# Kernel optimization log

Measured on AMD Instinct MI355X. Metric: run time of the kernel, lower is better.

## Reference

```python
import jax, jax.numpy as jnp
import numpy as np

B, S, D, H = 4, 1024, 1024, 16
DH = D // H


def setup_inputs() -> dict:
    key = jax.random.key(0)
    ks = jax.random.split(key, 9)
    s = 0.02
    return {
        "x": jax.random.normal(ks[0], (B, S, D), dtype=jnp.float32),
        "mask": jax.random.randint(ks[1], (B, 1, S), 0, 2, dtype=jnp.int32),
        "Wq": jax.random.normal(ks[2], (D, D), dtype=jnp.float32) * s,
        "bq": jnp.zeros((D,), dtype=jnp.float32),
        "Wk": jax.random.normal(ks[3], (D, D), dtype=jnp.float32) * s,
        "Wv": jax.random.normal(ks[4], (D, D), dtype=jnp.float32) * s,
        "bv": jnp.zeros((D,), dtype=jnp.float32),
        "Wo": jax.random.normal(ks[5], (D, D), dtype=jnp.float32) * s,
        "bo": jnp.zeros((D,), dtype=jnp.float32),
    }


def reference(x, mask, Wq, bq, Wk, Wv, bv, Wo, bo):
    # Linear projections (torch Linear: y = x @ W.T + b)
    q = x @ Wq.T + bq
    k = x @ Wk.T  # key has bias=False
    v = x @ Wv.T + bv

    scale = jnp.asarray(DH, x.dtype) ** (-0.25)
    # [B,S,D] -> [B,H,S,DH]
    qh = q.reshape(B, S, H, DH).transpose(0, 2, 1, 3) * scale
    kh = k.reshape(B, S, H, DH).transpose(0, 2, 1, 3) * scale
    vh = v.reshape(B, S, H, DH).transpose(0, 2, 1, 3)

    qk = jnp.einsum("bhqd,bhkd->bhqk", qh, kh)  # [B,H,S,S]

    # pad-mask branch: mask [B,1,S] -> [B,1,1,S], 0 means padded
    pad = (mask == 0)[:, :, None, :]
    min_value = jnp.finfo(qk.dtype).min
    qk = jnp.where(pad, min_value, qk)

    qk = qk.astype(jnp.float32)
    w = jax.nn.softmax(qk, axis=-1).astype(x.dtype)
    w = jnp.where(pad, jnp.asarray(0.0, w.dtype), w)

    wv = jnp.einsum("bhqk,bhkd->bhqd", w, vh)  # [B,H,S,DH]
    wv = wv.transpose(0, 2, 1, 3).reshape(B, S, D)
    out = wv @ Wo.T + bo
    return out, jax.lax.stop_gradient(qk)
```

## Files before the change

### kernel.cpp

```cpp
#include <hip/hip_runtime.h>

#define NB 4
#define NS 1024
#define ND 1024
#define NH 16
#define NDH 64

typedef __attribute__((ext_vector_type(8))) short short8;
typedef __attribute__((ext_vector_type(4))) short s16x4;
typedef __attribute__((ext_vector_type(4))) float f32x4;

#define SENT (-3.3895313892515355e38f)

static __device__ __forceinline__ unsigned short f2bf(float f) {
    unsigned u = __builtin_bit_cast(unsigned, f);
    u += 0x7fffu + ((u >> 16) & 1u);
    return (unsigned short)(u >> 16);
}

static __device__ __forceinline__ f32x4 mfma16(short8 a, short8 b, f32x4 c) {
    return __builtin_amdgcn_mfma_f32_16x16x32_bf16(a, b, c, 0, 0, 0);
}

typedef const __attribute__((address_space(1))) unsigned int gu32_t;
typedef __attribute__((address_space(3))) unsigned int su32_t;
#define GLOAD_LDS16(gp, lp) \
    __builtin_amdgcn_global_load_lds((gu32_t*)(const void*)(gp), (su32_t*)(void*)(lp), 16, 0, 0)

__global__ __launch_bounds__(256) void cast_to_bf16(
    const float* __restrict__ x,  const float* __restrict__ wq,
    const float* __restrict__ wk, const float* __restrict__ wv,
    const float* __restrict__ wo, short* __restrict__ xb,
    short* __restrict__ wqb, short* __restrict__ wkb,
    short* __restrict__ wvb, short* __restrict__ wob)
{
    int i = blockIdx.x * 256 + threadIdx.x;
    const float* s; short* d; int off;
    const int XQ = 1 << 20, WQ = 1 << 18;
    if (i < XQ)               { s = x;  d = xb;  off = i; }
    else if (i < XQ + WQ)     { s = wq; d = wqb; off = i - XQ; }
    else if (i < XQ + 2 * WQ) { s = wk; d = wkb; off = i - XQ - WQ; }
    else if (i < XQ + 3 * WQ) { s = wv; d = wvb; off = i - XQ - 2 * WQ; }
    else                      { s = wo; d = wob; off = i - XQ - 3 * WQ; }
    float4 v = ((const float4*)s)[off];
    s16x4 r = { (short)f2bf(v.x), (short)f2bf(v.y), (short)f2bf(v.z), (short)f2bf(v.w) };
    ((s16x4*)d)[off] = r;
}

__global__ __launch_bounds__(256) void gemm_qkv(
    const short* __restrict__ X, const short* __restrict__ Wq,
    const short* __restrict__ Wk, const short* __restrict__ Wv,
    const float* __restrict__ bq, const float* __restrict__ bv,
    short* __restrict__ qd, short* __restrict__ kd, short* __restrict__ vd)
{
    __shared__ short As[128 * 64];
    __shared__ short Bs[128 * 64];
    const int z = blockIdx.z;
    const short* W = (z == 0) ? Wq : (z == 1) ? Wk : Wv;
    const float* bias = (z == 0) ? bq : (z == 1) ? (const float*)nullptr : bv;
    const float scale = (z == 2) ? 1.0f : 0.35355339059327373f;
    short* dst = (z == 0) ? qd : (z == 1) ? kd : vd;

    const int tid = threadIdx.x;
    const int w = tid >> 6, l = tid & 63;
    const int lg = l >> 4, lc = l & 15;
    const int wr = w >> 1, wc = w & 1;
    const int bm = blockIdx.x, bn = blockIdx.y;
    const int K = ND;

    const f32x4 zf = {0.f, 0.f, 0.f, 0.f};
    f32x4 acc[4][4];
#pragma unroll
    for (int a = 0; a < 4; ++a)
#pragma unroll
        for (int b2 = 0; b2 < 4; ++b2) acc[a][b2] = zf;

    for (int t = 0; t < 16; ++t) {
        const int k0 = t * 64;
        __syncthreads();
#pragma unroll
        for (int i = 0; i < 4; ++i) {
            int lin = i * 256 + tid;
            int row = lin >> 3, cp = lin & 7;
            int c = cp ^ (row & 7);
            GLOAD_LDS16(X + (size_t)(bm * 128 + row) * K + k0 + c * 8, As + lin * 8);
            GLOAD_LDS16(W + (size_t)(bn * 128 + row) * K + k0 + c * 8, Bs + lin * 8);
        }
        __syncthreads();

        short8 af[4][2], bfr[4][2];
#pragma unroll
        for (int mb = 0; mb < 4; ++mb) {
            int r = wr * 64 + mb * 16 + lc;
#pragma unroll
            for (int ks = 0; ks < 2; ++ks) {
                int c = (ks * 4 + lg) ^ (r & 7);
                af[mb][ks] = *(const short8*)(As + r * 64 + c * 8);
            }
        }
#pragma unroll
        for (int nb = 0; nb < 4; ++nb) {
            int r = wc * 64 + nb * 16 + lc;
#pragma unroll
            for (int ks = 0; ks < 2; ++ks) {
                int c = (ks * 4 + lg) ^ (r & 7);
                bfr[nb][ks] = *(const short8*)(Bs + r * 64 + c * 8);
            }
        }
#pragma unroll
        for (int mb = 0; mb < 4; ++mb)
#pragma unroll
            for (int nb = 0; nb < 4; ++nb)
#pragma unroll
                for (int ks = 0; ks < 2; ++ks)
                    acc[mb][nb] = mfma16(af[mb][ks], bfr[nb][ks], acc[mb][nb]);
    }

#pragma unroll
    for (int mb = 0; mb < 4; ++mb) {
        int m0 = bm * 128 + wr * 64 + mb * 16 + lg * 4;
#pragma unroll
        for (int nb = 0; nb < 4; ++nb) {
            int n = bn * 128 + wc * 64 + nb * 16 + lc;
            float bv_ = bias ? bias[n] : 0.f;
#pragma unroll
            for (int r = 0; r < 4; ++r) {
                float v = (acc[mb][nb][r] + bv_) * scale;
                int mm = m0 + r;
                int b = mm >> 10, s = mm & 1023, h = n >> 6, d = n & 63;
                ((unsigned short*)dst)[(((size_t)(b * NH + h) * NS) + s) * NDH + d] = f2bf(v);
            }
        }
    }
}

__global__ __launch_bounds__(256) void gemm_out(
    const short* __restrict__ X, const short* __restrict__ W,
    const float* __restrict__ bias, float* __restrict__ outp)
{
    __shared__ short As[128 * 64];
    __shared__ short Bs[128 * 64];
    const int tid = threadIdx.x;
    const int w = tid >> 6, l = tid & 63;
    const int lg = l >> 4, lc = l & 15;
    const int wr = w >> 1, wc = w & 1;
    const int bm = blockIdx.x, bn = blockIdx.y;
    const int K = ND;

    const f32x4 zf = {0.f, 0.f, 0.f, 0.f};
    f32x4 acc[4][4];
#pragma unroll
    for (int a = 0; a < 4; ++a)
#pragma unroll
        for (int b2 = 0; b2 < 4; ++b2) acc[a][b2] = zf;

    for (int t = 0; t < 16; ++t) {
        const int k0 = t * 64;
        __syncthreads();
#pragma unroll
        for (int i = 0; i < 4; ++i) {
            int lin = i * 256 + tid;
            int row = lin >> 3, cp = lin & 7;
            int c = cp ^ (row & 7);
            GLOAD_LDS16(X + (size_t)(bm * 128 + row) * K + k0 + c * 8, As + lin * 8);
            GLOAD_LDS16(W + (size_t)(bn * 128 + row) * K + k0 + c * 8, Bs + lin * 8);
        }
        __syncthreads();

        short8 af[4][2], bfr[4][2];
#pragma unroll
        for (int mb = 0; mb < 4; ++mb) {
            int r = wr * 64 + mb * 16 + lc;
#pragma unroll
            for (int ks = 0; ks < 2; ++ks) {
                int c = (ks * 4 + lg) ^ (r & 7);
                af[mb][ks] = *(const short8*)(As + r * 64 + c * 8);
            }
        }
#pragma unroll
        for (int nb = 0; nb < 4; ++nb) {
            int r = wc * 64 + nb * 16 + lc;
#pragma unroll
            for (int ks = 0; ks < 2; ++ks) {
                int c = (ks * 4 + lg) ^ (r & 7);
                bfr[nb][ks] = *(const short8*)(Bs + r * 64 + c * 8);
            }
        }
#pragma unroll
        for (int mb = 0; mb < 4; ++mb)
#pragma unroll
            for (int nb = 0; nb < 4; ++nb)
#pragma unroll
                for (int ks = 0; ks < 2; ++ks)
                    acc[mb][nb] = mfma16(af[mb][ks], bfr[nb][ks], acc[mb][nb]);
    }

#pragma unroll
    for (int mb = 0; mb < 4; ++mb) {
        int m0 = bm * 128 + wr * 64 + mb * 16 + lg * 4;
#pragma unroll
        for (int nb = 0; nb < 4; ++nb) {
            int n = bn * 128 + wc * 64 + nb * 16 + lc;
            float bv_ = bias[n];
#pragma unroll
            for (int r = 0; r < 4; ++r)
                outp[(size_t)(m0 + r) * ND + n] = acc[mb][nb][r] + bv_;
        }
    }
}

__global__ __launch_bounds__(256) void transpose_v(
    const unsigned short* __restrict__ vb, unsigned short* __restrict__ vt)
{
    __shared__ unsigned short T[64][65];
    const int st = blockIdx.x, bh = blockIdx.y;
    const int tid = threadIdx.x;
#pragma unroll
    for (int i = 0; i < 2; ++i) {
        int lin = i * 256 + tid;
        int s = lin >> 3, dc = (lin & 7) * 8;
        short8 v = *(const short8*)(vb + ((size_t)(bh * NS + st * 64 + s)) * NDH + dc);
#pragma unroll
        for (int e = 0; e < 8; ++e) T[s][dc + e] = (unsigned short)v[e];
    }
    __syncthreads();
#pragma unroll
    for (int i = 0; i < 2; ++i) {
        int lin = i * 256 + tid;
        int d = lin >> 3, sc = (lin & 7) * 8;
        short8 v;
#pragma unroll
        for (int e = 0; e < 8; ++e) v[e] = (short)T[sc + e][d];
        *(short8*)(vt + ((size_t)(bh * NDH + d)) * NS + st * 64 + sc) = v;
    }
}

static __device__ __forceinline__ void stage_kv(
    const short* __restrict__ kb, const short* __restrict__ vt,
    int bh, int t, int tid, short* Ksb, short* Vsb)
{
#pragma unroll
    for (int i = 0; i < 2; ++i) {
        int lin = i * 256 + tid;
        int row = lin >> 3, cp = lin & 7;
        int c = cp ^ (row & 7);
        GLOAD_LDS16(kb + ((size_t)(bh * NS + t * 64 + row)) * NDH + c * 8, Ksb + lin * 8);
        GLOAD_LDS16(vt + ((size_t)(bh * NDH + row)) * NS + t * 64 + c * 8, Vsb + lin * 8);
    }
}

__global__ __launch_bounds__(256) void attn_mfma(
    const short* __restrict__ qb, const short* __restrict__ kb,
    const short* __restrict__ vt, const int* __restrict__ mask,
    float* __restrict__ qk_out, unsigned short* __restrict__ wv_out)
{
    __shared__ short Ks[2][64 * 64];
    __shared__ short Vs[2][64 * 64];
    __shared__ short Ps[4][16 * 68];
    __shared__ int Msk[NS];
    const int qt = blockIdx.x, bh = blockIdx.y;
    const int b = bh >> 4, h = bh & 15;
    const int q0 = qt * 64;
    const int tid = threadIdx.x;
    const int w = tid >> 6, l = tid & 63;
    const int lg = l >> 4, lc = l & 15;

#pragma unroll
    for (int i = 0; i < 4; ++i) Msk[i * 256 + tid] = mask[b * NS + i * 256 + tid];

    short8 aq[2];
    {
        const short* qrow = qb + ((size_t)(bh * NS + q0 + w * 16 + lc)) * NDH;
#pragma unroll
        for (int ks = 0; ks < 2; ++ks) aq[ks] = *(const short8*)(qrow + ks * 32 + lg * 8);
    }

    stage_kv(kb, vt, bh, 0, tid, Ks[0], Vs[0]);

    const f32x4 zf = {0.f, 0.f, 0.f, 0.f};
    f32x4 o[4];
    float mr[4], lr[4];
#pragma unroll
    for (int r = 0; r < 4; ++r) { mr[r] = -INFINITY; lr[r] = 0.f; }
#pragma unroll
    for (int db = 0; db < 4; ++db) o[db] = zf;

    __syncthreads();

    for (int t = 0; t < 16; ++t) {
        const int cur = t & 1;
        if (t < 15) stage_kv(kb, vt, bh, t + 1, tid, Ks[cur ^ 1], Vs[cur ^ 1]);
        const short* Ksc = Ks[cur];
        const short* Vsc = Vs[cur];

        f32x4 s[4];
#pragma unroll
        for (int jb = 0; jb < 4; ++jb) {
            s[jb] = zf;
#pragma unroll
            for (int ks = 0; ks < 2; ++ks) {
                int rk = jb * 16 + lc;
                int c = (ks * 4 + lg) ^ (rk & 7);
                short8 bk = *(const short8*)(Ksc + rk * 64 + c * 8);
                s[jb] = mfma16(aq[ks], bk, s[jb]);
            }
        }

        int mj[4];
#pragma unroll
        for (int jb = 0; jb < 4; ++jb) mj[jb] = Msk[t * 64 + jb * 16 + lc];

        const size_t qrb = (size_t)(bh * NS + q0 + w * 16 + lg * 4) * NS + t * 64 + lc;
#pragma unroll
        for (int jb = 0; jb < 4; ++jb)
#pragma unroll
            for (int r = 0; r < 4; ++r)
                qk_out[qrb + (size_t)r * NS + jb * 16] = mj[jb] ? s[jb][r] : SENT;

        float tm[4];
#pragma unroll
        for (int r = 0; r < 4; ++r) {
            float a0 = mj[0] ? s[0][r] : -INFINITY;
            float a1 = mj[1] ? s[1][r] : -INFINITY;
            float a2 = mj[2] ? s[2][r] : -INFINITY;
            float a3 = mj[3] ? s[3][r] : -INFINITY;
            tm[r] = fmaxf(fmaxf(a0, a1), fmaxf(a2, a3));
        }
#pragma unroll
        for (int off = 1; off <= 8; off <<= 1)
#pragma unroll
            for (int r = 0; r < 4; ++r) tm[r] = fmaxf(tm[r], __shfl_xor(tm[r], off, 16));

        float f[4], nm[4];
#pragma unroll
        for (int r = 0; r < 4; ++r) {
            nm[r] = fmaxf(mr[r], tm[r]);
            f[r] = (nm[r] == -INFINITY) ? 1.f : __expf(mr[r] - nm[r]);
            mr[r] = nm[r];
        }
        float p[4][4], ts[4] = {0.f, 0.f, 0.f, 0.f};
#pragma unroll
        for (int jb = 0; jb < 4; ++jb)
#pragma unroll
            for (int r = 0; r < 4; ++r) {
                float e = mj[jb] ? __expf(s[jb][r] - nm[r]) : 0.f;
                p[jb][r] = e;
                ts[r] += e;
            }
#pragma unroll
        for (int off = 1; off <= 8; off <<= 1)
#pragma unroll
            for (int r = 0; r < 4; ++r) ts[r] += __shfl_xor(ts[r], off, 16);
        f32x4 fv = {f[0], f[1], f[2], f[3]};
#pragma unroll
        for (int r = 0; r < 4; ++r) lr[r] = lr[r] * f[r] + ts[r];
#pragma unroll
        for (int db = 0; db < 4; ++db) o[db] *= fv;

#pragma unroll
        for (int jb = 0; jb < 4; ++jb)
#pragma unroll
            for (int r = 0; r < 4; ++r)
                Ps[w][(lg * 4 + r) * 68 + jb * 16 + lc] = (short)f2bf(p[jb][r]);
        short8 pa[2];
#pragma unroll
        for (int ks = 0; ks < 2; ++ks)
            pa[ks] = *(const short8*)(&Ps[w][lc * 68 + ks * 32 + lg * 8]);

#pragma unroll
        for (int db = 0; db < 4; ++db)
#pragma unroll
            for (int ks = 0; ks < 2; ++ks) {
                int rv = db * 16 + lc;
                int c = (ks * 4 + lg) ^ (rv & 7);
                short8 bv = *(const short8*)(Vsc + rv * 64 + c * 8);
                o[db] = mfma16(pa[ks], bv, o[db]);
            }

        __syncthreads();
    }

    float inv[4];
#pragma unroll
    for (int r = 0; r < 4; ++r) inv[r] = (lr[r] > 0.f) ? 1.f / lr[r] : 0.f;
#pragma unroll
    for (int db = 0; db < 4; ++db)
#pragma unroll
        for (int r = 0; r < 4; ++r) {
            float v = o[db][r] * inv[r];
            wv_out[(((size_t)(b * NS + q0 + w * 16 + lg * 4 + r)) * NH + h) * NDH + db * 16 + lc] =
                f2bf(v);
        }
}

extern "C" void kernel_launch(void* const* d_in, const int* in_sizes, int n_in,
                              void* d_out, int out_size, void* d_ws, size_t ws_size,
                              hipStream_t stream) {
    const float* x    = (const float*)d_in[0];
    const int*   mask = (const int*)d_in[1];
    const float* Wq   = (const float*)d_in[2];
    const float* bq   = (const float*)d_in[3];
    const float* Wk   = (const float*)d_in[4];
    const float* Wv   = (const float*)d_in[5];
    const float* bv   = (const float*)d_in[6];
    const float* Wo   = (const float*)d_in[7];
    const float* bo   = (const float*)d_in[8];

    float* out    = (float*)d_out;
    float* qk_out = out + (size_t)NB * NS * ND;

    const size_t MI = 1u << 20;
    short* xb  = (short*)d_ws;
    short* wqb = xb  + 4 * MI;
    short* wkb = wqb + MI;
    short* wvb = wkb + MI;
    short* wob = wvb + MI;
    short* qbf = wob + MI;
    short* kbf = qbf + 4 * MI;
    short* vbf = kbf + 4 * MI;
    short* vtb = vbf + 4 * MI;
    short* wvo = vtb + 4 * MI;

    cast_to_bf16<<<8192, 256, 0, stream>>>(x, Wq, Wk, Wv, Wo, xb, wqb, wkb, wvb, wob);

    dim3 blk(256);
    dim3 qgrid(32, 8, 3);
    gemm_qkv<<<qgrid, blk, 0, stream>>>(xb, wqb, wkb, wvb, bq, bv, qbf, kbf, vbf);

    dim3 tgrid(16, 64);
    transpose_v<<<tgrid, blk, 0, stream>>>((const unsigned short*)vbf, (unsigned short*)vtb);

    dim3 agrid(16, 64);
    attn_mfma<<<agrid, blk, 0, stream>>>(qbf, kbf, vtb, mask, qk_out, (unsigned short*)wvo);

    dim3 ogrid(32, 8);
    gemm_out<<<ogrid, blk, 0, stream>>>(wvo, wob, bo, out);
}
```

Before: 431.8 us.

## Fuse V transpose into QKV GEMM, double-buffer out GEMM, transpose QK^T fragments

The QKV GEMM epilogue now writes V directly in transposed [b,h,d,s] layout with packed 4-element stores, which removes the separate transpose_v kernel and its extra round trip through global memory. The output GEMM gains LDS double buffering so the next K-tile loads while the current one is multiplied. In the attention kernel the score MFMA operands are swapped so each lane holds 4 consecutive key columns. That allows vectorized nontemporal float4 stores of the large qk output, int4 mask loads and a single running max/sum per lane. The cost is a doubled LDS footprint in gemm_out and cross-lane shuffles to broadcast the rescale factors.

```diff
diff --git a/kernel.cpp b/kernel.cpp
--- a/kernel.cpp
+++ b/kernel.cpp
@@ -51,7 +51,7 @@
     const short* __restrict__ X, const short* __restrict__ Wq,
     const short* __restrict__ Wk, const short* __restrict__ Wv,
     const float* __restrict__ bq, const float* __restrict__ bv,
-    short* __restrict__ qd, short* __restrict__ kd, short* __restrict__ vd)
+    short* __restrict__ qd, short* __restrict__ kd, short* __restrict__ vtd)
 {
     __shared__ short As[128 * 64];
     __shared__ short Bs[128 * 64];
@@ -59,7 +59,6 @@
     const short* W = (z == 0) ? Wq : (z == 1) ? Wk : Wv;
     const float* bias = (z == 0) ? bq : (z == 1) ? (const float*)nullptr : bv;
     const float scale = (z == 2) ? 1.0f : 0.35355339059327373f;
-    short* dst = (z == 0) ? qd : (z == 1) ? kd : vd;
 
     const int tid = threadIdx.x;
     const int w = tid >> 6, l = tid & 63;
@@ -119,33 +118,88 @@
 #pragma unroll
     for (int mb = 0; mb < 4; ++mb) {
         int m0 = bm * 128 + wr * 64 + mb * 16 + lg * 4;
+        int b = m0 >> 10, s0 = m0 & 1023;
 #pragma unroll
         for (int nb = 0; nb < 4; ++nb) {
             int n = bn * 128 + wc * 64 + nb * 16 + lc;
+            int h = (n >> 6) & 15, d = n & 63;
             float bv_ = bias ? bias[n] : 0.f;
-#pragma unroll
-            for (int r = 0; r < 4; ++r) {
-                float v = (acc[mb][nb][r] + bv_) * scale;
-                int mm = m0 + r;
-                int b = mm >> 10, s = mm & 1023, h = n >> 6, d = n & 63;
-                ((unsigned short*)dst)[(((size_t)(b * NH + h) * NS) + s) * NDH + d] = f2bf(v);
-            }
-        }
-    }
+            if (z == 2) {
+                s16x4 pk;
+#pragma unroll
+                for (int r = 0; r < 4; ++r) pk[r] = (short)f2bf(acc[mb][nb][r] + bv_);
+                *(s16x4*)(vtd + (((size_t)(b * NH + h) * NDH + d) * NS + s0)) = pk;
+            } else {
+                short* dst = (z == 0) ? qd : kd;
+#pragma unroll
+                for (int r = 0; r < 4; ++r) {
+                    float v = (acc[mb][nb][r] + bv_) * scale;
+                    ((unsigned short*)dst)[(((size_t)(b * NH + h) * NS) + s0 + r) * NDH + d] =
+                        f2bf(v);
+                }
+            }
+        }
+    }
+}
+
+static __device__ __forceinline__ void stage_ab(
+    const short* __restrict__ X, const short* __restrict__ W,
+    int bm, int bn, int t, int tid, short* Asb, short* Bsb)
+{
+    const int k0 = t * 64;
+#pragma unroll
+    for (int i = 0; i < 4; ++i) {
+        int lin = i * 256 + tid;
+        int row = lin >> 3, cp = lin & 7;
+        int c = cp ^ (row & 7);
+        GLOAD_LDS16(X + (size_t)(bm * 128 + row) * ND + k0 + c * 8, Asb + lin * 8);
+        GLOAD_LDS16(W + (size_t)(bn * 128 + row) * ND + k0 + c * 8, Bsb + lin * 8);
+    }
+}
+
+static __device__ __forceinline__ void kstep128(
+    const short* Asb, const short* Bsb, int wr, int wc, int lg, int lc,
+    f32x4 acc[4][4])
+{
+    short8 af[4][2], bfr[4][2];
+#pragma unroll
+    for (int mb = 0; mb < 4; ++mb) {
+        int r = wr * 64 + mb * 16 + lc;
+#pragma unroll
+        for (int ks = 0; ks < 2; ++ks) {
+            int c = (ks * 4 + lg) ^ (r & 7);
+            af[mb][ks] = *(const short8*)(Asb + r * 64 + c * 8);
+        }
+    }
+#pragma unroll
+    for (int nb = 0; nb < 4; ++nb) {
+        int r = wc * 64 + nb * 16 + lc;
+#pragma unroll
+        for (int ks = 0; ks < 2; ++ks) {
+            int c = (ks * 4 + lg) ^ (r & 7);
+            bfr[nb][ks] = *(const short8*)(Bsb + r * 64 + c * 8);
+        }
+    }
+#pragma unroll
+    for (int mb = 0; mb < 4; ++mb)
+#pragma unroll
+        for (int nb = 0; nb < 4; ++nb)
+#pragma unroll
+            for (int ks = 0; ks < 2; ++ks)
+                acc[mb][nb] = mfma16(af[mb][ks], bfr[nb][ks], acc[mb][nb]);
 }
 
 __global__ __launch_bounds__(256) void gemm_out(
     const short* __restrict__ X, const short* __restrict__ W,
     const float* __restrict__ bias, float* __restrict__ outp)
 {
-    __shared__ short As[128 * 64];
-    __shared__ short Bs[128 * 64];
+    __shared__ short As0[128 * 64], As1[128 * 64];
+    __shared__ short Bs0[128 * 64], Bs1[128 * 64];
     const int tid = threadIdx.x;
     const int w = tid >> 6, l = tid & 63;
     const int lg = l >> 4, lc = l & 15;
     const int wr = w >> 1, wc = w & 1;
     const int bm = blockIdx.x, bn = blockIdx.y;
-    const int K = ND;
 
     const f32x4 zf = {0.f, 0.f, 0.f, 0.f};
     f32x4 acc[4][4];
@@ -154,45 +208,15 @@
 #pragma unroll
         for (int b2 = 0; b2 < 4; ++b2) acc[a][b2] = zf;
 
-    for (int t = 0; t < 16; ++t) {
-        const int k0 = t * 64;
+    stage_ab(X, W, bm, bn, 0, tid, As0, Bs0);
+    __syncthreads();
+    for (int t = 0; t < 16; t += 2) {
+        if (t + 1 < 16) stage_ab(X, W, bm, bn, t + 1, tid, As1, Bs1);
+        kstep128(As0, Bs0, wr, wc, lg, lc, acc);
         __syncthreads();
-#pragma unroll
-        for (int i = 0; i < 4; ++i) {
-            int lin = i * 256 + tid;
-            int row = lin >> 3, cp = lin & 7;
-            int c = cp ^ (row & 7);
-            GLOAD_LDS16(X + (size_t)(bm * 128 + row) * K + k0 + c * 8, As + lin * 8);
-            GLOAD_LDS16(W + (size_t)(bn * 128 + row) * K + k0 + c * 8, Bs + lin * 8);
-        }
+        if (t + 2 < 16) stage_ab(X, W, bm, bn, t + 2, tid, As0, Bs0);
+        kstep128(As1, Bs1, wr, wc, lg, lc, acc);
         __syncthreads();
-
-        short8 af[4][2], bfr[4][2];
-#pragma unroll
-        for (int mb = 0; mb < 4; ++mb) {
-            int r = wr * 64 + mb * 16 + lc;
-#pragma unroll
-            for (int ks = 0; ks < 2; ++ks) {
-                int c = (ks * 4 + lg) ^ (r & 7);
-                af[mb][ks] = *(const short8*)(As + r * 64 + c * 8);
-            }
-        }
-#pragma unroll
-        for (int nb = 0; nb < 4; ++nb) {
-            int r = wc * 64 + nb * 16 + lc;
-#pragma unroll
-            for (int ks = 0; ks < 2; ++ks) {
-                int c = (ks * 4 + lg) ^ (r & 7);
-                bfr[nb][ks] = *(const short8*)(Bs + r * 64 + c * 8);
-            }
-        }
-#pragma unroll
-        for (int mb = 0; mb < 4; ++mb)
-#pragma unroll
-            for (int nb = 0; nb < 4; ++nb)
-#pragma unroll
-                for (int ks = 0; ks < 2; ++ks)
-                    acc[mb][nb] = mfma16(af[mb][ks], bfr[nb][ks], acc[mb][nb]);
     }
 
 #pragma unroll
@@ -206,32 +230,6 @@
             for (int r = 0; r < 4; ++r)
                 outp[(size_t)(m0 + r) * ND + n] = acc[mb][nb][r] + bv_;
         }
-    }
-}
-
-__global__ __launch_bounds__(256) void transpose_v(
-    const unsigned short* __restrict__ vb, unsigned short* __restrict__ vt)
-{
-    __shared__ unsigned short T[64][65];
-    const int st = blockIdx.x, bh = blockIdx.y;
-    const int tid = threadIdx.x;
-#pragma unroll
-    for (int i = 0; i < 2; ++i) {
-        int lin = i * 256 + tid;
-        int s = lin >> 3, dc = (lin & 7) * 8;
-        short8 v = *(const short8*)(vb + ((size_t)(bh * NS + st * 64 + s)) * NDH + dc);
-#pragma unroll
-        for (int e = 0; e < 8; ++e) T[s][dc + e] = (unsigned short)v[e];
-    }
-    __syncthreads();
-#pragma unroll
-    for (int i = 0; i < 2; ++i) {
-        int lin = i * 256 + tid;
-        int d = lin >> 3, sc = (lin & 7) * 8;
-        short8 v;
-#pragma unroll
-        for (int e = 0; e < 8; ++e) v[e] = (short)T[sc + e][d];
-        *(short8*)(vt + ((size_t)(bh * NDH + d)) * NS + st * 64 + sc) = v;
     }
 }
 
@@ -254,8 +252,8 @@
     const short* __restrict__ vt, const int* __restrict__ mask,
     float* __restrict__ qk_out, unsigned short* __restrict__ wv_out)
 {
-    __shared__ short Ks[2][64 * 64];
-    __shared__ short Vs[2][64 * 64];
+    __shared__ short Ks0[64 * 64], Ks1[64 * 64];
+    __shared__ short Vs0[64 * 64], Vs1[64 * 64];
     __shared__ short Ps[4][16 * 68];
     __shared__ int Msk[NS];
     const int qt = blockIdx.x, bh = blockIdx.y;
@@ -275,119 +273,124 @@
         for (int ks = 0; ks < 2; ++ks) aq[ks] = *(const short8*)(qrow + ks * 32 + lg * 8);
     }
 
-    stage_kv(kb, vt, bh, 0, tid, Ks[0], Vs[0]);
-
     const f32x4 zf = {0.f, 0.f, 0.f, 0.f};
     f32x4 o[4];
-    float mr[4], lr[4];
-#pragma unroll
-    for (int r = 0; r < 4; ++r) { mr[r] = -INFINITY; lr[r] = 0.f; }
+    float mr = -INFINITY, lr = 0.f;
 #pragma unroll
     for (int db = 0; db < 4; ++db) o[db] = zf;
 
+    const size_t qrowbase = (size_t)(bh * NS + q0 + w * 16 + lc) * NS;
+
+    stage_kv(kb, vt, bh, 0, tid, Ks0, Vs0);
     __syncthreads();
 
-    for (int t = 0; t < 16; ++t) {
-        const int cur = t & 1;
-        if (t < 15) stage_kv(kb, vt, bh, t + 1, tid, Ks[cur ^ 1], Vs[cur ^ 1]);
-        const short* Ksc = Ks[cur];
-        const short* Vsc = Vs[cur];
-
-        f32x4 s[4];
-#pragma unroll
-        for (int jb = 0; jb < 4; ++jb) {
-            s[jb] = zf;
-#pragma unroll
-            for (int ks = 0; ks < 2; ++ks) {
-                int rk = jb * 16 + lc;
-                int c = (ks * 4 + lg) ^ (rk & 7);
-                short8 bk = *(const short8*)(Ksc + rk * 64 + c * 8);
-                s[jb] = mfma16(aq[ks], bk, s[jb]);
-            }
-        }
-
-        int mj[4];
-#pragma unroll
-        for (int jb = 0; jb < 4; ++jb) mj[jb] = Msk[t * 64 + jb * 16 + lc];
-
-        const size_t qrb = (size_t)(bh * NS + q0 + w * 16 + lg * 4) * NS + t * 64 + lc;
-#pragma unroll
-        for (int jb = 0; jb < 4; ++jb)
-#pragma unroll
-            for (int r = 0; r < 4; ++r)
-                qk_out[qrb + (size_t)r * NS + jb * 16] = mj[jb] ? s[jb][r] : SENT;
-
-        float tm[4];
+#pragma unroll
+    for (int t2 = 0; t2 < 16; t2 += 2) {
+#pragma unroll
+        for (int half = 0; half < 2; ++half) {
+            const int t = t2 + half;
+            const short* Ksc = half ? Ks1 : Ks0;
+            const short* Vsc = half ? Vs1 : Vs0;
+            if (t + 1 < 16)
+                stage_kv(kb, vt, bh, t + 1, tid, half ? Ks0 : Ks1, half ? Vs0 : Vs1);
+
+            f32x4 s[4];
+#pragma unroll
+            for (int jb = 0; jb < 4; ++jb) {
+                s[jb] = zf;
+#pragma unroll
+                for (int ks = 0; ks < 2; ++ks) {
+                    int rk = jb * 16 + lc;
+                    int c = (ks * 4 + lg) ^ (rk & 7);
+                    short8 kf = *(const short8*)(Ksc + rk * 64 + c * 8);
+                    s[jb] = mfma16(kf, aq[ks], s[jb]);
+                }
+            }
+
+            float sm[4][4];
+#pragma unroll
+            for (int jb = 0; jb < 4; ++jb) {
+                int4 mi = *(const int4*)(Msk + t * 64 + jb * 16 + lg * 4);
+                f32x4 sv;
+                sv[0] = mi.x ? s[jb][0] : SENT;
+                sv[1] = mi.y ? s[jb][1] : SENT;
+                sv[2] = mi.z ? s[jb][2] : SENT;
+                sv[3] = mi.w ? s[jb][3] : SENT;
+                __builtin_nontemporal_store(
+                    sv, (f32x4*)(qk_out + qrowbase + t * 64 + jb * 16 + lg * 4));
+                sm[jb][0] = mi.x ? s[jb][0] : -INFINITY;
+                sm[jb][1] = mi.y ? s[jb][1] : -INFINITY;
+                sm[jb][2] = mi.z ? s[jb][2] : -INFINITY;
+                sm[jb][3] = mi.w ? s[jb][3] : -INFINITY;
+            }
+
+            float pm = -INFINITY;
+#pragma unroll
+            for (int jb = 0; jb < 4; ++jb)
+                pm = fmaxf(pm, fmaxf(fmaxf(sm[jb][0], sm[jb][1]),
+                                     fmaxf(sm[jb][2], sm[jb][3])));
+            pm = fmaxf(pm, __shfl_xor(pm, 16));
+            pm = fmaxf(pm, __shfl_xor(pm, 32));
+
+            float nm = fmaxf(mr, pm);
+            float f = (nm == -INFINITY) ? 1.f : __expf(mr - nm);
+            float nms = (nm == -INFINITY) ? 0.f : nm;
+            mr = nm;
+
+            float p[4][4], ps = 0.f;
+#pragma unroll
+            for (int jb = 0; jb < 4; ++jb)
+#pragma unroll
+                for (int r = 0; r < 4; ++r) {
+                    float e = __expf(sm[jb][r] - nms);
+                    p[jb][r] = e;
+                    ps += e;
+                }
+            ps += __shfl_xor(ps, 16);
+            ps += __shfl_xor(ps, 32);
+            lr = lr * f + ps;
+
+            f32x4 fv;
+#pragma unroll
+            for (int r = 0; r < 4; ++r) fv[r] = __shfl(f, lg * 4 + r, 16);
+#pragma unroll
+            for (int db = 0; db < 4; ++db) o[db] *= fv;
+
+#pragma unroll
+            for (int jb = 0; jb < 4; ++jb) {
+                s16x4 pk;
+#pragma unroll
+                for (int r = 0; r < 4; ++r) pk[r] = (short)f2bf(p[jb][r]);
+                *(s16x4*)(&Ps[w][lc * 68 + jb * 16 + lg * 4]) = pk;
+            }
+            short8 pa[2];
+#pragma unroll
+            for (int ks = 0; ks < 2; ++ks)
+                pa[ks] = *(const short8*)(&Ps[w][lc * 68 + ks * 32 + lg * 8]);
+
+#pragma unroll
+            for (int db = 0; db < 4; ++db)
+#pragma unroll
+                for (int ks = 0; ks < 2; ++ks) {
+                    int rv = db * 16 + lc;
+                    int c = (ks * 4 + lg) ^ (rv & 7);
+                    short8 bvf = *(const short8*)(Vsc + rv * 64 + c * 8);
+                    o[db] = mfma16(pa[ks], bvf, o[db]);
+                }
+
+            __syncthreads();
+        }
+    }
+
+    float inv = (lr > 0.f) ? 1.f / lr : 0.f;
+    f32x4 invv;
+#pragma unroll
+    for (int r = 0; r < 4; ++r) invv[r] = __shfl(inv, lg * 4 + r, 16);
+#pragma unroll
+    for (int db = 0; db < 4; ++db)
 #pragma unroll
         for (int r = 0; r < 4; ++r) {
-            float a0 = mj[0] ? s[0][r] : -INFINITY;
-            float a1 = mj[1] ? s[1][r] : -INFINITY;
-            float a2 = mj[2] ? s[2][r] : -INFINITY;
-            float a3 = mj[3] ? s[3][r] : -INFINITY;
-            tm[r] = fmaxf(fmaxf(a0, a1), fmaxf(a2, a3));
-        }
-#pragma unroll
-        for (int off = 1; off <= 8; off <<= 1)
-#pragma unroll
-            for (int r = 0; r < 4; ++r) tm[r] = fmaxf(tm[r], __shfl_xor(tm[r], off, 16));
-
-        float f[4], nm[4];
-#pragma unroll
-        for (int r = 0; r < 4; ++r) {
-            nm[r] = fmaxf(mr[r], tm[r]);
-            f[r] = (nm[r] == -INFINITY) ? 1.f : __expf(mr[r] - nm[r]);
-            mr[r] = nm[r];
-        }
-        float p[4][4], ts[4] = {0.f, 0.f, 0.f, 0.f};
-#pragma unroll
-        for (int jb = 0; jb < 4; ++jb)
-#pragma unroll
-            for (int r = 0; r < 4; ++r) {
-                float e = mj[jb] ? __expf(s[jb][r] - nm[r]) : 0.f;
-                p[jb][r] = e;
-                ts[r] += e;
-            }
-#pragma unroll
-        for (int off = 1; off <= 8; off <<= 1)
-#pragma unroll
-            for (int r = 0; r < 4; ++r) ts[r] += __shfl_xor(ts[r], off, 16);
-        f32x4 fv = {f[0], f[1], f[2], f[3]};
-#pragma unroll
-        for (int r = 0; r < 4; ++r) lr[r] = lr[r] * f[r] + ts[r];
-#pragma unroll
-        for (int db = 0; db < 4; ++db) o[db] *= fv;
-
-#pragma unroll
-        for (int jb = 0; jb < 4; ++jb)
-#pragma unroll
-            for (int r = 0; r < 4; ++r)
-                Ps[w][(lg * 4 + r) * 68 + jb * 16 + lc] = (short)f2bf(p[jb][r]);
-        short8 pa[2];
-#pragma unroll
-        for (int ks = 0; ks < 2; ++ks)
-            pa[ks] = *(const short8*)(&Ps[w][lc * 68 + ks * 32 + lg * 8]);
-
-#pragma unroll
-        for (int db = 0; db < 4; ++db)
-#pragma unroll
-            for (int ks = 0; ks < 2; ++ks) {
-                int rv = db * 16 + lc;
-                int c = (ks * 4 + lg) ^ (rv & 7);
-                short8 bv = *(const short8*)(Vsc + rv * 64 + c * 8);
-                o[db] = mfma16(pa[ks], bv, o[db]);
-            }
-
-        __syncthreads();
-    }
-
-    float inv[4];
-#pragma unroll
-    for (int r = 0; r < 4; ++r) inv[r] = (lr[r] > 0.f) ? 1.f / lr[r] : 0.f;
-#pragma unroll
-    for (int db = 0; db < 4; ++db)
-#pragma unroll
-        for (int r = 0; r < 4; ++r) {
-            float v = o[db][r] * inv[r];
+            float v = o[db][r] * invv[r];
             wv_out[(((size_t)(b * NS + q0 + w * 16 + lg * 4 + r)) * NH + h) * NDH + db * 16 + lc] =
                 f2bf(v);
         }
@@ -417,18 +420,14 @@
     short* wob = wvb + MI;
     short* qbf = wob + MI;
     short* kbf = qbf + 4 * MI;
-    short* vbf = kbf + 4 * MI;
-    short* vtb = vbf + 4 * MI;
+    short* vtb = kbf + 4 * MI;
     short* wvo = vtb + 4 * MI;
 
     cast_to_bf16<<<8192, 256, 0, stream>>>(x, Wq, Wk, Wv, Wo, xb, wqb, wkb, wvb, wob);
 
     dim3 blk(256);
     dim3 qgrid(32, 8, 3);
-    gemm_qkv<<<qgrid, blk, 0, stream>>>(xb, wqb, wkb, wvb, bq, bv, qbf, kbf, vbf);
-
-    dim3 tgrid(16, 64);
-    transpose_v<<<tgrid, blk, 0, stream>>>((const unsigned short*)vbf, (unsigned short*)vtb);
+    gemm_qkv<<<qgrid, blk, 0, stream>>>(xb, wqb, wkb, wvb, bq, bv, qbf, kbf, vtb);
 
     dim3 agrid(16, 64);
     attn_mfma<<<agrid, blk, 0, stream>>>(qbf, kbf, vtb, mask, qk_out, (unsigned short*)wvo);
```

After: 421.4 us. 1.02x faster.
